# Performance work log

Measured on AMD Instinct MI355X. Metric: run time of the kernel, lower is better.

The kernel has to match this reference:

```python
import jax, jax.numpy as jnp
import numpy as np

IN_DIM, DIM, HEADS = 128, 32, 4
L, B = 256, 1


def setup_inputs() -> dict:
    key = jax.random.key(0)
    ks = jax.random.split(key, 10)
    z = jax.random.normal(ks[0], (B, L, L, IN_DIM), dtype=jnp.float32)
    src_mask = jax.random.randint(ks[1], (B, L), 0, 2, dtype=jnp.int32)
    s = 1.0 / np.sqrt(IN_DIM)
    return {
        "z": z,
        "ln_gamma": jnp.ones((IN_DIM,), jnp.float32),
        "ln_beta": jnp.zeros((IN_DIM,), jnp.float32),
        "w_qkv": jax.random.normal(ks[2], (IN_DIM, 3 * HEADS * DIM), jnp.float32) * s,
        "w_pair": jax.random.normal(ks[3], (IN_DIM, HEADS), jnp.float32) * s,
        "w_gate": jax.random.normal(ks[4], (IN_DIM, IN_DIM), jnp.float32) * s,
        "b_gate": jax.random.normal(ks[5], (IN_DIM,), jnp.float32) * 0.02,
        "w_out": jax.random.normal(ks[6], (HEADS * DIM, IN_DIM), jnp.float32) * s,
        "b_out": jax.random.normal(ks[7], (IN_DIM,), jnp.float32) * 0.02,
        "src_mask": src_mask,
    }


def reference(z, ln_gamma, ln_beta, w_qkv, w_pair, w_gate, b_gate, w_out, b_out, src_mask):
    b, i, j, c = z.shape
    h, d = HEADS, DIM
    # mask: zeros -> -1, then outer product -> [b, L, L]
    m = jnp.where(src_mask == 0, -1, src_mask).astype(z.dtype)
    attn_mask = m[:, :, None] * m[:, None, :]
    # LayerNorm over channel dim (eps=1e-5, as nn.LayerNorm default)
    mu = jnp.mean(z, axis=-1, keepdims=True)
    var = jnp.mean((z - mu) ** 2, axis=-1, keepdims=True)
    zn = (z - mu) * jax.lax.rsqrt(var + 1e-5) * ln_gamma + ln_beta
    # qkv projection (no bias), split into heads
    qkv = zn @ w_qkv  # [b,i,j,3*h*d]
    q, k, v = jnp.split(qkv, 3, axis=-1)
    q = q.reshape(b, i, j, h, d)
    k = k.reshape(b, i, j, h, d)
    v = v.reshape(b, i, j, h, d)
    bias = zn @ w_pair  # [b,i,j,h]
    gate = jax.nn.sigmoid(zn @ w_gate + b_gate)  # [b,i,j,c]
    scale = jnp.asarray(d, z.dtype) ** 0.5
    # row-wise attention: attend along j within each row r=i
    logits = jnp.einsum('brihd,brjhd->brijh', q, k) / scale + bias[:, None]
    logits = jnp.where(attn_mask[:, None, :, :, None] == -1, jnp.asarray(-1e-9, z.dtype), logits)
    attn = jax.nn.softmax(logits, axis=3)
    out = jnp.einsum('brijh,brjhd->brihd', attn, v).reshape(b, i, j, h * d)
    out = gate * out
    return out @ w_out + b_out
```

## Files before the change

kernel.cpp:

```cpp
#include <hip/hip_runtime.h>
#include <hip/hip_bf16.h>
#include <math.h>

typedef __attribute__((ext_vector_type(4))) short short4v;
typedef __attribute__((ext_vector_type(8))) short short8v;
typedef __attribute__((ext_vector_type(4))) float f32x4;

#define QB_OFF    0
#define KB_OFF    16777216
#define VB_OFF    33554432
#define BIAS_OFF  50331648
#define GATEB_OFF 51380224
#define ATTB_OFF  68157440
#define WT_OFF    84934656
#define WOT_OFF   85065728

static __device__ __forceinline__ short f2bf(float x) {
    __hip_bfloat16 h = __float2bfloat16(x);
    return *reinterpret_cast<short*>(&h);
}
static __device__ __forceinline__ float bf2f(short x) {
    __hip_bfloat16 h = *reinterpret_cast<__hip_bfloat16*>(&x);
    return __bfloat162float(h);
}

__global__ __launch_bounds__(128) void k_prep_w(
    const float* __restrict__ w_qkv, const float* __restrict__ w_gate,
    const float* __restrict__ w_out, __hip_bfloat16* __restrict__ wT,
    __hip_bfloat16* __restrict__ woT)
{
    const int n = blockIdx.x, k = threadIdx.x;
    if (n < 384)      wT[n*128 + k]        = __float2bfloat16(w_qkv[k*384 + n]);
    else if (n < 512) wT[n*128 + k]        = __float2bfloat16(w_gate[k*128 + (n-384)]);
    else              woT[(n-512)*128 + k] = __float2bfloat16(w_out[k*128 + (n-512)]);
}

__global__ __launch_bounds__(256) void k1_ln_proj(
    const float* __restrict__ z, const float* __restrict__ gamma,
    const float* __restrict__ beta, const float* __restrict__ w_pair,
    const float* __restrict__ b_gate, const int* __restrict__ src_mask,
    const __hip_bfloat16* __restrict__ wT,
    __hip_bfloat16* __restrict__ qb, __hip_bfloat16* __restrict__ kb,
    __hip_bfloat16* __restrict__ vb, float* __restrict__ biasf,
    __hip_bfloat16* __restrict__ gateb)
{
    const int tid = threadIdx.x;
    const int lane = tid & 63, wv = tid >> 6;
    const int l15 = lane & 15, lg4 = lane >> 4;
    const int half = blockIdx.x >> 9;
    const int tokbase = (blockIdx.x & 511) * 128 + wv * 32;

    float zn[2][32];
    float s[2] = {0.f, 0.f}, s2[2] = {0.f, 0.f};
    #pragma unroll
    for (int mt = 0; mt < 2; ++mt) {
        const float* zp = z + (size_t)(tokbase + mt*16 + l15) * 128 + lg4*8;
        #pragma unroll
        for (int ks = 0; ks < 4; ++ks) {
            float4 a = *(const float4*)(zp + ks*32);
            float4 b = *(const float4*)(zp + ks*32 + 4);
            zn[mt][ks*8+0] = a.x; zn[mt][ks*8+1] = a.y;
            zn[mt][ks*8+2] = a.z; zn[mt][ks*8+3] = a.w;
            zn[mt][ks*8+4] = b.x; zn[mt][ks*8+5] = b.y;
            zn[mt][ks*8+6] = b.z; zn[mt][ks*8+7] = b.w;
            s[mt]  += a.x + a.y + a.z + a.w + b.x + b.y + b.z + b.w;
            s2[mt] += a.x*a.x + a.y*a.y + a.z*a.z + a.w*a.w
                    + b.x*b.x + b.y*b.y + b.z*b.z + b.w*b.w;
        }
    }
    #pragma unroll
    for (int mt = 0; mt < 2; ++mt) {
        s[mt]  += __shfl_xor(s[mt], 16);  s[mt]  += __shfl_xor(s[mt], 32);
        s2[mt] += __shfl_xor(s2[mt], 16); s2[mt] += __shfl_xor(s2[mt], 32);
    }

    #pragma unroll
    for (int ks = 0; ks < 4; ++ks) {
        float4 g0 = *(const float4*)(gamma + ks*32 + lg4*8);
        float4 g1 = *(const float4*)(gamma + ks*32 + lg4*8 + 4);
        float4 b0 = *(const float4*)(beta  + ks*32 + lg4*8);
        float4 b1 = *(const float4*)(beta  + ks*32 + lg4*8 + 4);
        float gg[8] = {g0.x,g0.y,g0.z,g0.w,g1.x,g1.y,g1.z,g1.w};
        float bb[8] = {b0.x,b0.y,b0.z,b0.w,b1.x,b1.y,b1.z,b1.w};
        #pragma unroll
        for (int mt = 0; mt < 2; ++mt) {
            const float mu  = s[mt] * (1.f/128.f);
            const float inv = rsqrtf(s2[mt]*(1.f/128.f) - mu*mu + 1e-5f);
            #pragma unroll
            for (int e = 0; e < 8; ++e)
                zn[mt][ks*8+e] = (zn[mt][ks*8+e] - mu) * inv * gg[e] + bb[e];
        }
    }

    if (half == 0) {
        float pr[2][4] = {{0,0,0,0},{0,0,0,0}};
        #pragma unroll
        for (int ks = 0; ks < 4; ++ks)
            #pragma unroll
            for (int e = 0; e < 8; ++e) {
                float4 wp = *(const float4*)(w_pair + (ks*32 + lg4*8 + e)*4);
                #pragma unroll
                for (int mt = 0; mt < 2; ++mt) {
                    const float a = zn[mt][ks*8+e];
                    pr[mt][0] = fmaf(a, wp.x, pr[mt][0]);
                    pr[mt][1] = fmaf(a, wp.y, pr[mt][1]);
                    pr[mt][2] = fmaf(a, wp.z, pr[mt][2]);
                    pr[mt][3] = fmaf(a, wp.w, pr[mt][3]);
                }
            }
        #pragma unroll
        for (int mt = 0; mt < 2; ++mt)
            #pragma unroll
            for (int h = 0; h < 4; ++h) {
                pr[mt][h] += __shfl_xor(pr[mt][h], 16);
                pr[mt][h] += __shfl_xor(pr[mt][h], 32);
            }
        if (lg4 == 0) {
            #pragma unroll
            for (int mt = 0; mt < 2; ++mt) {
                const int t = tokbase + mt*16 + l15;
                const int i = t >> 8, j = t & 255;
                const bool masked = (src_mask[i] == 0) != (src_mask[j] == 0);
                #pragma unroll
                for (int h = 0; h < 4; ++h)
                    biasf[(size_t)(h*256 + i)*256 + j] = masked ? 1e30f : pr[mt][h];
            }
        }
    }

    short8v afr[2][4];
    #pragma unroll
    for (int mt = 0; mt < 2; ++mt)
        #pragma unroll
        for (int ks = 0; ks < 4; ++ks) {
            short8v f;
            #pragma unroll
            for (int e = 0; e < 8; ++e) f[e] = f2bf(zn[mt][ks*8+e]);
            afr[mt][ks] = f;
        }

    const ushort* wTu = (const ushort*)wT;
    for (int ci = 0; ci < 4; ++ci) {
        const int ch = half*4 + ci;
        f32x4 acc[2][4];
        #pragma unroll
        for (int mt = 0; mt < 2; ++mt)
            #pragma unroll
            for (int nt = 0; nt < 4; ++nt) acc[mt][nt] = (f32x4){0.f,0.f,0.f,0.f};
        const ushort* Bb = wTu + (size_t)ch * 64 * 128;
        #pragma unroll
        for (int ks = 0; ks < 4; ++ks)
            #pragma unroll
            for (int nt = 0; nt < 4; ++nt) {
                short8v bfr = *(const short8v*)(Bb + (nt*16 + l15)*128 + ks*32 + lg4*8);
                acc[0][nt] = __builtin_amdgcn_mfma_f32_16x16x32_bf16(afr[0][ks], bfr, acc[0][nt], 0,0,0);
                acc[1][nt] = __builtin_amdgcn_mfma_f32_16x16x32_bf16(afr[1][ks], bfr, acc[1][nt], 0,0,0);
            }
        if (ch < 6) {
            __hip_bfloat16* dst = (ch < 2 ? qb : (ch < 4 ? kb : vb));
            #pragma unroll
            for (int mt = 0; mt < 2; ++mt)
                #pragma unroll
                for (int nt = 0; nt < 4; ++nt) {
                    const int nh = (ch & 1)*64 + nt*16 + l15;
                    const int h = nh >> 5, d = nh & 31;
                    #pragma unroll
                    for (int e = 0; e < 4; ++e) {
                        const int t = tokbase + mt*16 + lg4*4 + e;
                        const int i = t >> 8, j = t & 255;
                        dst[(size_t)((i*4 + h)*256 + j)*32 + d] = __float2bfloat16(acc[mt][nt][e]);
                    }
                }
        } else {
            #pragma unroll
            for (int mt = 0; mt < 2; ++mt)
                #pragma unroll
                for (int nt = 0; nt < 4; ++nt) {
                    const int c = (ch - 6)*64 + nt*16 + l15;
                    const float bg = b_gate[c];
                    #pragma unroll
                    for (int e = 0; e < 4; ++e) {
                        const int t = tokbase + mt*16 + lg4*4 + e;
                        const float v = 1.f / (1.f + __expf(-(acc[mt][nt][e] + bg)));
                        gateb[(size_t)t*128 + c] = __float2bfloat16(v);
                    }
                }
        }
    }
}

__global__ __launch_bounds__(256) void k_attn_mfma(
    const __hip_bfloat16* __restrict__ qb_, const __hip_bfloat16* __restrict__ kb_,
    const __hip_bfloat16* __restrict__ vb_, const float* __restrict__ biasf,
    __hip_bfloat16* __restrict__ attb)
{
    __shared__ __align__(16) char klds[256 * 80];
    __shared__ __align__(16) char vlds[16384];
    const int tid  = threadIdx.x;
    const int lane = tid & 63;
    const int wv   = tid >> 6;
    const int h = blockIdx.x >> 8, r = blockIdx.x & 255;
    const int rh = r * 4 + h;
    const int l15 = lane & 15, lg4 = lane >> 4;

    const ushort* qg = (const ushort*)qb_ + (size_t)rh * 8192;
    const ushort* kg = (const ushort*)kb_ + (size_t)rh * 8192;
    const ushort* vg = (const ushort*)vb_ + (size_t)rh * 8192;

    #pragma unroll
    for (int t = 0; t < 4; ++t) {
        uint4 kv = *(const uint4*)(kg + t*2048 + tid*8);
        *(uint4*)(klds + (t*64 + (tid >> 2))*80 + (tid & 3)*16) = kv;
    }
    {
        const int j = tid;
        uint4 tmp[4];
        #pragma unroll
        for (int c = 0; c < 4; ++c)
            tmp[c] = *(const uint4*)(vg + (size_t)j*32 + c*8);
        const ushort* vals = (const ushort*)tmp;
        #pragma unroll
        for (int d = 0; d < 32; ++d)
            *(ushort*)(vlds + d*512 + (((j >> 2) ^ (d & 15)) << 3) + (j & 3)*2) = vals[d];
    }
    __syncthreads();

    const float inv_scale = 0.17677669529663687f;

    for (int ii = 0; ii < 4; ++ii) {
        const int it = wv*4 + ii;
        short8v qf = *(const short8v*)(qg + (it*16 + l15)*32 + lg4*8);

        f32x4 s[16];
        #pragma unroll
        for (int jt = 0; jt < 16; ++jt) {
            short8v kf = *(const short8v*)(klds + (jt*16 + l15)*80 + lg4*16);
            s[jt] = __builtin_amdgcn_mfma_f32_16x16x32_bf16(
                        kf, qf, (f32x4){0.f,0.f,0.f,0.f}, 0, 0, 0);
        }

        const float* bp = biasf + (size_t)(h*256 + it*16 + l15) * 256;
        #pragma unroll
        for (int jt = 0; jt < 16; ++jt) {
            f32x4 bv = *(const f32x4*)(bp + jt*16 + lg4*4);
            #pragma unroll
            for (int e = 0; e < 4; ++e)
                s[jt][e] = (bv[e] > 1e29f) ? -1e-9f : fmaf(s[jt][e], inv_scale, bv[e]);
        }

        float m = -INFINITY;
        #pragma unroll
        for (int jt = 0; jt < 16; ++jt) {
            const float a = fmaxf(fmaxf(s[jt][0], s[jt][1]),
                                  fmaxf(s[jt][2], s[jt][3]));
            m = fmaxf(m, a);
        }
        m = fmaxf(m, __shfl_xor(m, 16));
        m = fmaxf(m, __shfl_xor(m, 32));

        float lsum = 0.f;
        #pragma unroll
        for (int jt = 0; jt < 16; ++jt)
            #pragma unroll
            for (int e = 0; e < 4; ++e) {
                const float p = __expf(s[jt][e] - m);
                s[jt][e] = p;
                lsum += p;
            }
        lsum += __shfl_xor(lsum, 16);
        lsum += __shfl_xor(lsum, 32);
        const float invl = 1.f / lsum;

        short4v pa[16];
        #pragma unroll
        for (int jt = 0; jt < 16; ++jt) {
            short4v t4;
            t4[0] = f2bf(s[jt][0] * invl); t4[1] = f2bf(s[jt][1] * invl);
            t4[2] = f2bf(s[jt][2] * invl); t4[3] = f2bf(s[jt][3] * invl);
            pa[jt] = t4;
        }

        f32x4 o0 = {0.f,0.f,0.f,0.f}, o1 = {0.f,0.f,0.f,0.f};
        #pragma unroll
        for (int jt = 0; jt < 16; ++jt) {
            const int d0 = l15, d1 = 16 + l15;
            short4v vf0 = *(const short4v*)(vlds + d0*512 + (((jt*4 + lg4) ^ (d0 & 15)) << 3));
            short4v vf1 = *(const short4v*)(vlds + d1*512 + (((jt*4 + lg4) ^ (d1 & 15)) << 3));
            o0 = __builtin_amdgcn_mfma_f32_16x16x16bf16_1k(pa[jt], vf0, o0, 0, 0, 0);
            o1 = __builtin_amdgcn_mfma_f32_16x16x16bf16_1k(pa[jt], vf1, o1, 0, 0, 0);
        }

        __hip_bfloat16* op = attb + ((size_t)(r*256 + it*16) * 128) + h*32;
        #pragma unroll
        for (int e = 0; e < 4; ++e) {
            op[(lg4*4 + e)*128 +      l15] = __float2bfloat16(o0[e]);
            op[(lg4*4 + e)*128 + 16 + l15] = __float2bfloat16(o1[e]);
        }
    }
}

__global__ __launch_bounds__(256) void k3_out_proj(
    const __hip_bfloat16* __restrict__ gateb, const __hip_bfloat16* __restrict__ attb,
    const __hip_bfloat16* __restrict__ woT, const float* __restrict__ b_out,
    float* __restrict__ out)
{
    const int tid = threadIdx.x;
    const int lane = tid & 63, wv = tid >> 6;
    const int l15 = lane & 15, lg4 = lane >> 4;
    const int tokbase = blockIdx.x * 64 + wv * 16;

    const ushort* gu = (const ushort*)gateb;
    const ushort* au = (const ushort*)attb;

    short8v afr[4];
    #pragma unroll
    for (int ks = 0; ks < 4; ++ks) {
        const size_t base = (size_t)(tokbase + l15)*128 + ks*32 + lg4*8;
        short8v gv = *(const short8v*)(gu + base);
        short8v av = *(const short8v*)(au + base);
        short8v p;
        #pragma unroll
        for (int e = 0; e < 8; ++e) p[e] = f2bf(bf2f(gv[e]) * bf2f(av[e]));
        afr[ks] = p;
    }

    const ushort* wo = (const ushort*)woT;
    for (int ch = 0; ch < 2; ++ch) {
        f32x4 acc[4];
        #pragma unroll
        for (int nt = 0; nt < 4; ++nt) acc[nt] = (f32x4){0.f,0.f,0.f,0.f};
        const ushort* Bb = wo + (size_t)ch * 64 * 128;
        #pragma unroll
        for (int ks = 0; ks < 4; ++ks)
            #pragma unroll
            for (int nt = 0; nt < 4; ++nt) {
                short8v bfr = *(const short8v*)(Bb + (nt*16 + l15)*128 + ks*32 + lg4*8);
                acc[nt] = __builtin_amdgcn_mfma_f32_16x16x32_bf16(afr[ks], bfr, acc[nt], 0,0,0);
            }
        #pragma unroll
        for (int nt = 0; nt < 4; ++nt) {
            const int n = ch*64 + nt*16 + l15;
            const float bo = b_out[n];
            #pragma unroll
            for (int e = 0; e < 4; ++e) {
                const int t = tokbase + lg4*4 + e;
                out[(size_t)t*128 + n] = acc[nt][e] + bo;
            }
        }
    }
}

extern "C" void kernel_launch(void* const* d_in, const int* in_sizes, int n_in,
                              void* d_out, int out_size, void* d_ws, size_t ws_size,
                              hipStream_t stream)
{
    const float* z       = (const float*)d_in[0];
    const float* gamma   = (const float*)d_in[1];
    const float* beta    = (const float*)d_in[2];
    const float* w_qkv   = (const float*)d_in[3];
    const float* w_pair  = (const float*)d_in[4];
    const float* w_gate  = (const float*)d_in[5];
    const float* b_gate  = (const float*)d_in[6];
    const float* w_out   = (const float*)d_in[7];
    const float* b_out   = (const float*)d_in[8];
    const int*   src_mask= (const int*)d_in[9];
    float* out = (float*)d_out;
    char*  wsb = (char*)d_ws;

    __hip_bfloat16* qb    = (__hip_bfloat16*)(wsb + QB_OFF);
    __hip_bfloat16* kb    = (__hip_bfloat16*)(wsb + KB_OFF);
    __hip_bfloat16* vb    = (__hip_bfloat16*)(wsb + VB_OFF);
    float*          biasf = (float*)(wsb + BIAS_OFF);
    __hip_bfloat16* gateb = (__hip_bfloat16*)(wsb + GATEB_OFF);
    __hip_bfloat16* attb  = (__hip_bfloat16*)(wsb + ATTB_OFF);
    __hip_bfloat16* wT    = (__hip_bfloat16*)(wsb + WT_OFF);
    __hip_bfloat16* woT   = (__hip_bfloat16*)(wsb + WOT_OFF);

    hipLaunchKernelGGL(k_prep_w, dim3(640), dim3(128), 0, stream,
                       w_qkv, w_gate, w_out, wT, woT);
    hipLaunchKernelGGL(k1_ln_proj, dim3(1024), dim3(256), 0, stream,
                       z, gamma, beta, w_pair, b_gate, src_mask, wT,
                       qb, kb, vb, biasf, gateb);
    hipLaunchKernelGGL(k_attn_mfma, dim3(1024), dim3(256), 0, stream,
                       qb, kb, vb, biasf, attb);
    hipLaunchKernelGGL(k3_out_proj, dim3(1024), dim3(256), 0, stream,
                       gateb, attb, woT, b_out, out);
}
```

Before: 138.0 us.

## Swap MFMA operands for packed vector stores, merge k1 halves, register V fragments

Swaps the A/B operands of the MFMAs so each lane holds four consecutive output columns, which lets q/k/v, gate, attention output and the final projection be written with packed 8- or 16-byte stores instead of scattered 2-byte stores. The LayerNorm/projection kernel no longer splits channels across two block halves, so each block computes LN once and does all eight channel chunks. This removes the duplicated z reads and LN work. The attention kernel drops to 128 threads and keeps V fragments in registers instead of a transposed LDS copy, which trades LDS traffic for much higher register pressure and possibly lower occupancy.

Measured after the change: 128.6 us, median of 2. -6.8%, faster.

```diff
diff --git a/kernel.cpp b/kernel.cpp
--- a/kernel.cpp
+++ b/kernel.cpp
@@ -23,6 +23,10 @@
     __hip_bfloat16 h = *reinterpret_cast<__hip_bfloat16*>(&x);
     return __bfloat162float(h);
 }
+static __device__ __forceinline__ unsigned int pk2(float a, float b) {
+    return (unsigned int)(unsigned short)f2bf(a)
+         | ((unsigned int)(unsigned short)f2bf(b) << 16);
+}
 
 __global__ __launch_bounds__(128) void k_prep_w(
     const float* __restrict__ w_qkv, const float* __restrict__ w_gate,
@@ -47,8 +51,7 @@
     const int tid = threadIdx.x;
     const int lane = tid & 63, wv = tid >> 6;
     const int l15 = lane & 15, lg4 = lane >> 4;
-    const int half = blockIdx.x >> 9;
-    const int tokbase = (blockIdx.x & 511) * 128 + wv * 32;
+    const int tokbase = blockIdx.x * 128 + wv * 32;
 
     float zn[2][32];
     float s[2] = {0.f, 0.f}, s2[2] = {0.f, 0.f};
@@ -92,7 +95,7 @@
         }
     }
 
-    if (half == 0) {
+    {
         float pr[2][4] = {{0,0,0,0},{0,0,0,0}};
         #pragma unroll
         for (int ks = 0; ks < 4; ++ks)
@@ -140,8 +143,7 @@
         }
 
     const ushort* wTu = (const ushort*)wT;
-    for (int ci = 0; ci < 4; ++ci) {
-        const int ch = half*4 + ci;
+    for (int ch = 0; ch < 8; ++ch) {
         f32x4 acc[2][4];
         #pragma unroll
         for (int mt = 0; mt < 2; ++mt)
@@ -153,49 +155,55 @@
             #pragma unroll
             for (int nt = 0; nt < 4; ++nt) {
                 short8v bfr = *(const short8v*)(Bb + (nt*16 + l15)*128 + ks*32 + lg4*8);
-                acc[0][nt] = __builtin_amdgcn_mfma_f32_16x16x32_bf16(afr[0][ks], bfr, acc[0][nt], 0,0,0);
-                acc[1][nt] = __builtin_amdgcn_mfma_f32_16x16x32_bf16(afr[1][ks], bfr, acc[1][nt], 0,0,0);
+                acc[0][nt] = __builtin_amdgcn_mfma_f32_16x16x32_bf16(bfr, afr[0][ks], acc[0][nt], 0,0,0);
+                acc[1][nt] = __builtin_amdgcn_mfma_f32_16x16x32_bf16(bfr, afr[1][ks], acc[1][nt], 0,0,0);
             }
         if (ch < 6) {
-            __hip_bfloat16* dst = (ch < 2 ? qb : (ch < 4 ? kb : vb));
-            #pragma unroll
-            for (int mt = 0; mt < 2; ++mt)
+            __hip_bfloat16* dstb = (ch < 2 ? qb : (ch < 4 ? kb : vb));
+            ushort* dst = (ushort*)dstb;
+            #pragma unroll
+            for (int mt = 0; mt < 2; ++mt) {
+                const int t = tokbase + mt*16 + l15;
+                const int i = t >> 8, j = t & 255;
                 #pragma unroll
                 for (int nt = 0; nt < 4; ++nt) {
-                    const int nh = (ch & 1)*64 + nt*16 + l15;
-                    const int h = nh >> 5, d = nh & 31;
-                    #pragma unroll
-                    for (int e = 0; e < 4; ++e) {
-                        const int t = tokbase + mt*16 + lg4*4 + e;
-                        const int i = t >> 8, j = t & 255;
-                        dst[(size_t)((i*4 + h)*256 + j)*32 + d] = __float2bfloat16(acc[mt][nt][e]);
-                    }
+                    const int h  = (ch & 1)*2 + (nt >> 1);
+                    const int d0 = (nt & 1)*16 + lg4*4;
+                    uint2 v;
+                    v.x = pk2(acc[mt][nt][0], acc[mt][nt][1]);
+                    v.y = pk2(acc[mt][nt][2], acc[mt][nt][3]);
+                    *(uint2*)(dst + ((size_t)((i*4 + h)*256 + j))*32 + d0) = v;
                 }
+            }
         } else {
-            #pragma unroll
-            for (int mt = 0; mt < 2; ++mt)
+            ushort* gdst = (ushort*)gateb;
+            #pragma unroll
+            for (int mt = 0; mt < 2; ++mt) {
+                const int t = tokbase + mt*16 + l15;
                 #pragma unroll
                 for (int nt = 0; nt < 4; ++nt) {
-                    const int c = (ch - 6)*64 + nt*16 + l15;
-                    const float bg = b_gate[c];
-                    #pragma unroll
-                    for (int e = 0; e < 4; ++e) {
-                        const int t = tokbase + mt*16 + lg4*4 + e;
-                        const float v = 1.f / (1.f + __expf(-(acc[mt][nt][e] + bg)));
-                        gateb[(size_t)t*128 + c] = __float2bfloat16(v);
-                    }
+                    const int c0 = (ch - 6)*64 + nt*16 + lg4*4;
+                    float4 bg = *(const float4*)(b_gate + c0);
+                    const float g0 = 1.f / (1.f + __expf(-(acc[mt][nt][0] + bg.x)));
+                    const float g1 = 1.f / (1.f + __expf(-(acc[mt][nt][1] + bg.y)));
+                    const float g2 = 1.f / (1.f + __expf(-(acc[mt][nt][2] + bg.z)));
+                    const float g3 = 1.f / (1.f + __expf(-(acc[mt][nt][3] + bg.w)));
+                    uint2 v;
+                    v.x = pk2(g0, g1);
+                    v.y = pk2(g2, g3);
+                    *(uint2*)(gdst + (size_t)t*128 + c0) = v;
                 }
-        }
-    }
-}
-
-__global__ __launch_bounds__(256) void k_attn_mfma(
+            }
+        }
+    }
+}
+
+__global__ __launch_bounds__(128) void k_attn_mfma(
     const __hip_bfloat16* __restrict__ qb_, const __hip_bfloat16* __restrict__ kb_,
     const __hip_bfloat16* __restrict__ vb_, const float* __restrict__ biasf,
     __hip_bfloat16* __restrict__ attb)
 {
     __shared__ __align__(16) char klds[256 * 80];
-    __shared__ __align__(16) char vlds[16384];
     const int tid  = threadIdx.x;
     const int lane = tid & 63;
     const int wv   = tid >> 6;
@@ -207,28 +215,29 @@
     const ushort* kg = (const ushort*)kb_ + (size_t)rh * 8192;
     const ushort* vg = (const ushort*)vb_ + (size_t)rh * 8192;
 
-    #pragma unroll
-    for (int t = 0; t < 4; ++t) {
-        uint4 kv = *(const uint4*)(kg + t*2048 + tid*8);
-        *(uint4*)(klds + (t*64 + (tid >> 2))*80 + (tid & 3)*16) = kv;
-    }
-    {
-        const int j = tid;
-        uint4 tmp[4];
-        #pragma unroll
-        for (int c = 0; c < 4; ++c)
-            tmp[c] = *(const uint4*)(vg + (size_t)j*32 + c*8);
-        const ushort* vals = (const ushort*)tmp;
-        #pragma unroll
-        for (int d = 0; d < 32; ++d)
-            *(ushort*)(vlds + d*512 + (((j >> 2) ^ (d & 15)) << 3) + (j & 3)*2) = vals[d];
+    short4v vfrag[16][2];
+    #pragma unroll
+    for (int jt = 0; jt < 16; ++jt)
+        #pragma unroll
+        for (int dt = 0; dt < 2; ++dt) {
+            short4v f;
+            #pragma unroll
+            for (int e = 0; e < 4; ++e)
+                f[e] = (short)vg[(size_t)(jt*16 + lg4*4 + e)*32 + dt*16 + l15];
+            vfrag[jt][dt] = f;
+        }
+
+    #pragma unroll
+    for (int t = 0; t < 8; ++t) {
+        uint4 kv = *(const uint4*)(kg + t*1024 + tid*8);
+        *(uint4*)(klds + (t*32 + (tid >> 2))*80 + (tid & 3)*16) = kv;
     }
     __syncthreads();
 
     const float inv_scale = 0.17677669529663687f;
 
-    for (int ii = 0; ii < 4; ++ii) {
-        const int it = wv*4 + ii;
+    for (int ii = 0; ii < 8; ++ii) {
+        const int it = wv*8 + ii;
         short8v qf = *(const short8v*)(qg + (it*16 + l15)*32 + lg4*8);
 
         f32x4 s[16];
@@ -283,19 +292,16 @@
         f32x4 o0 = {0.f,0.f,0.f,0.f}, o1 = {0.f,0.f,0.f,0.f};
         #pragma unroll
         for (int jt = 0; jt < 16; ++jt) {
-            const int d0 = l15, d1 = 16 + l15;
-            short4v vf0 = *(const short4v*)(vlds + d0*512 + (((jt*4 + lg4) ^ (d0 & 15)) << 3));
-            short4v vf1 = *(const short4v*)(vlds + d1*512 + (((jt*4 + lg4) ^ (d1 & 15)) << 3));
-            o0 = __builtin_amdgcn_mfma_f32_16x16x16bf16_1k(pa[jt], vf0, o0, 0, 0, 0);
-            o1 = __builtin_amdgcn_mfma_f32_16x16x16bf16_1k(pa[jt], vf1, o1, 0, 0, 0);
-        }
-
-        __hip_bfloat16* op = attb + ((size_t)(r*256 + it*16) * 128) + h*32;
-        #pragma unroll
-        for (int e = 0; e < 4; ++e) {
-            op[(lg4*4 + e)*128 +      l15] = __float2bfloat16(o0[e]);
-            op[(lg4*4 + e)*128 + 16 + l15] = __float2bfloat16(o1[e]);
-        }
+            o0 = __builtin_amdgcn_mfma_f32_16x16x16bf16_1k(vfrag[jt][0], pa[jt], o0, 0, 0, 0);
+            o1 = __builtin_amdgcn_mfma_f32_16x16x16bf16_1k(vfrag[jt][1], pa[jt], o1, 0, 0, 0);
+        }
+
+        ushort* op = (ushort*)attb + (size_t)(r*256 + it*16 + l15)*128 + h*32 + lg4*4;
+        uint2 v0, v1;
+        v0.x = pk2(o0[0], o0[1]); v0.y = pk2(o0[2], o0[3]);
+        v1.x = pk2(o1[0], o1[1]); v1.y = pk2(o1[2], o1[3]);
+        *(uint2*)(op)      = v0;
+        *(uint2*)(op + 16) = v1;
     }
 }
 
@@ -325,6 +331,7 @@
     }
 
     const ushort* wo = (const ushort*)woT;
+    const int t = tokbase + l15;
     for (int ch = 0; ch < 2; ++ch) {
         f32x4 acc[4];
         #pragma unroll
@@ -335,17 +342,18 @@
             #pragma unroll
             for (int nt = 0; nt < 4; ++nt) {
                 short8v bfr = *(const short8v*)(Bb + (nt*16 + l15)*128 + ks*32 + lg4*8);
-                acc[nt] = __builtin_amdgcn_mfma_f32_16x16x32_bf16(afr[ks], bfr, acc[nt], 0,0,0);
+                acc[nt] = __builtin_amdgcn_mfma_f32_16x16x32_bf16(bfr, afr[ks], acc[nt], 0,0,0);
             }
         #pragma unroll
         for (int nt = 0; nt < 4; ++nt) {
-            const int n = ch*64 + nt*16 + l15;
-            const float bo = b_out[n];
-            #pragma unroll
-            for (int e = 0; e < 4; ++e) {
-                const int t = tokbase + lg4*4 + e;
-                out[(size_t)t*128 + n] = acc[nt][e] + bo;
-            }
+            const int n0 = ch*64 + nt*16 + lg4*4;
+            float4 bo = *(const float4*)(b_out + n0);
+            float4 v;
+            v.x = acc[nt][0] + bo.x;
+            v.y = acc[nt][1] + bo.y;
+            v.z = acc[nt][2] + bo.z;
+            v.w = acc[nt][3] + bo.w;
+            *(float4*)(out + (size_t)t*128 + n0) = v;
         }
     }
 }
@@ -378,10 +386,10 @@
 
     hipLaunchKernelGGL(k_prep_w, dim3(640), dim3(128), 0, stream,
                        w_qkv, w_gate, w_out, wT, woT);
-    hipLaunchKernelGGL(k1_ln_proj, dim3(1024), dim3(256), 0, stream,
+    hipLaunchKernelGGL(k1_ln_proj, dim3(512), dim3(256), 0, stream,
                        z, gamma, beta, w_pair, b_gate, src_mask, wT,
                        qb, kb, vb, biasf, gateb);
-    hipLaunchKernelGGL(k_attn_mfma, dim3(1024), dim3(256), 0, stream,
+    hipLaunchKernelGGL(k_attn_mfma, dim3(1024), dim3(128), 0, stream,
                        qb, kb, vb, biasf, attb);
     hipLaunchKernelGGL(k3_out_proj, dim3(1024), dim3(256), 0, stream,
                        gateb, attb, woT, b_out, out);
```
